# Performance work log

Hardware: AMD Instinct MI355X
Metric: run time of the kernel (lower is better)

Reference implementation:

```python
import jax, jax.numpy as jnp
import numpy as np

C = 256
CQK = C // 8  # query/key projection dim


def setup_inputs() -> dict:
    key = jax.random.key(0)
    ks = jax.random.split(key, 8)
    B, H, W = 4, 64, 64
    x = jax.random.normal(ks[0], (B, C, H, W), dtype=jnp.float32)
    # 1x1 Conv1d == per-position linear: weight [out, in], bias [out]
    Wq = jax.random.normal(ks[1], (CQK, C), dtype=jnp.float32) * (1.0 / np.sqrt(C))
    bq = jax.random.normal(ks[2], (CQK,), dtype=jnp.float32) * 0.01
    Wk = jax.random.normal(ks[3], (CQK, C), dtype=jnp.float32) * (1.0 / np.sqrt(C))
    bk = jax.random.normal(ks[4], (CQK,), dtype=jnp.float32) * 0.01
    Wv = jax.random.normal(ks[5], (C, C), dtype=jnp.float32) * (1.0 / np.sqrt(C))
    bv = jax.random.normal(ks[6], (C,), dtype=jnp.float32) * 0.01
    gamma = jax.random.normal(ks[7], (1,), dtype=jnp.float32) * 0.1
    return {"x": x, "Wq": Wq, "bq": bq, "Wk": Wk, "bk": bk,
            "Wv": Wv, "bv": bv, "gamma": gamma}


def reference(x, Wq, bq, Wk, bk, Wv, bv, gamma):
    B, Cc, H, W = x.shape
    xf = x.reshape(B, Cc, H * W)                      # [B, C, N]
    q = jnp.einsum('oc,bcn->bon', Wq, xf) + bq[:, None]   # [B, C/8, N]
    k = jnp.einsum('oc,bcn->bon', Wk, xf) + bk[:, None]   # [B, C/8, N]
    v = jnp.einsum('oc,bcn->bon', Wv, xf) + bv[:, None]   # [B, C,   N]
    # energy = q^T k  (unscaled, SAGAN-style)
    energy = jnp.einsum('bon,bom->bnm', q, k)              # [B, N, N]
    attn = jax.nn.softmax(energy, axis=-1)                 # rows over key dim
    # out = value @ attention^T
    out = jnp.einsum('bcm,bnm->bcn', v, attn)              # [B, C, N]
    out = out.reshape(B, Cc, H, W)
    return gamma * out + x
```

## Files before the change

### kernel.cpp

```cpp
#include <hip/hip_runtime.h>
#include <hip/hip_bf16.h>
#include <math.h>
#include <stdint.h>

#define N_POS 4096
#define C_DIM 256
#define CQK_D 32
#define NSPLIT 3

typedef __attribute__((ext_vector_type(8))) short bf16x8;
typedef __attribute__((ext_vector_type(4))) float f32x4;
typedef __attribute__((ext_vector_type(4))) uint32_t u32x4;

__device__ inline uint16_t f2bf(float f){
  union { __hip_bfloat16 h; uint16_t u; } c;
  c.h = __float2bfloat16(f);
  return c.u;
}
__device__ inline uint32_t pk2bf(float a, float b){
  union { __hip_bfloat162 h; uint32_t u; } c;
  c.h = __float22bfloat162_rn(float2{a, b});
  return c.u;
}
__device__ inline float bf2f_lo(uint32_t d){ return __uint_as_float(d << 16); }
__device__ inline float bf2f_hi(uint32_t d){ return __uint_as_float(d & 0xFFFF0000u); }

__global__ __launch_bounds__(256) void prep(
    const float* __restrict__ x,
    const float* __restrict__ Wq, const float* __restrict__ bq,
    const float* __restrict__ Wk, const float* __restrict__ bk,
    const float* __restrict__ Wv, const float* __restrict__ bv,
    ushort* __restrict__ xT_bf, ushort* __restrict__ W_bf, float* __restrict__ bias_f)
{
    const int tid = threadIdx.x;
    if (blockIdx.x == 64) {
        const int sub = blockIdx.z * 4 + blockIdx.y;
        const int e0 = sub * 5120;
        #pragma unroll
        for (int it = 0; it < 5; ++it) {
            const int e = e0 + (it*256 + tid)*4;
            const int o = e >> 8, c = e & 255;
            float4 w;
            if (o < 32)       w = *reinterpret_cast<const float4*>(&Wq[o*C_DIM + c]);
            else if (o < 64)  w = *reinterpret_cast<const float4*>(&Wk[(o-32)*C_DIM + c]);
            else              w = *reinterpret_cast<const float4*>(&Wv[(o-64)*C_DIM + c]);
            uint2 u; u.x = pk2bf(w.x, w.y); u.y = pk2bf(w.z, w.w);
            *reinterpret_cast<uint2*>(W_bf + e) = u;
        }
        if (sub == 0) {
            for (int i = tid; i < 320; i += 256)
                bias_f[i] = (i < 32) ? bq[i] : (i < 64) ? bk[i-32] : bv[i-64];
        }
        return;
    }
    __shared__ float t[64][65];
    const int jj4 = (tid & 15) * 4;
    const int rg  = tid >> 4;
    const int n0 = blockIdx.x * 64;
    const int c0 = blockIdx.y * 64;
    const int b  = blockIdx.z;
    #pragma unroll
    for (int ii = 0; ii < 4; ++ii) {
        const int cl = ii*16 + rg;
        const float4 xv = *reinterpret_cast<const float4*>(
            &x[((size_t)(b*C_DIM) + c0 + cl)*N_POS + n0 + jj4]);
        float* tr = &t[cl][jj4];
        tr[0] = xv.x; tr[1] = xv.y; tr[2] = xv.z; tr[3] = xv.w;
    }
    __syncthreads();
    #pragma unroll
    for (int ii = 0; ii < 8; ++ii) {
        const int flat = ii*256 + tid;
        const int nl = flat >> 5;
        const int cp = flat & 31;
        const uint32_t d = pk2bf(t[2*cp][nl], t[2*cp+1][nl]);
        *reinterpret_cast<uint32_t*>(xT_bf + ((size_t)(b*N_POS) + n0 + nl)*C_DIM + c0 + 2*cp) = d;
    }
}

__global__ __launch_bounds__(256, 4) void qkv_gemm(
    const ushort* __restrict__ xT_bf, const ushort* __restrict__ W_bf,
    const float* __restrict__ bias_f,
    ushort* __restrict__ q_bf, ushort* __restrict__ k_bf, ushort* __restrict__ v_bf)
{
    __shared__ ushort xs[64*C_DIM];
    const int tid  = threadIdx.x;
    const int wv   = tid >> 6;
    const int lane = tid & 63;
    const int g    = lane >> 4;
    const int q    = lane & 15;
    const int y    = blockIdx.y;
    const int b    = blockIdx.z;
    const int n0   = blockIdx.x * 64;

    {
        const char* xTb = (const char*)(xT_bf + ((size_t)(b*N_POS) + n0)*C_DIM);
        const int n_l    = (tid*16) >> 9;
        const int inner  = (tid & 31) << 4;
        #pragma unroll
        for (int s = 0; s < 8; ++s) {
            const int n = s*8 + n_l;
            const int src_inner = inner ^ ((n & 7) << 4);
            __builtin_amdgcn_global_load_lds(
                (const __attribute__((address_space(1))) uint32_t*)(xTb + (size_t)n*512 + src_inner),
                (__attribute__((address_space(3))) uint32_t*)((char*)xs + s*4096 + wv*1024),
                16, 0, 0);
        }
    }
    __syncthreads();

    f32x4 zero4 = {0.f,0.f,0.f,0.f};
    f32x4 acc[5];
    #pragma unroll
    for (int i = 0; i < 5; ++i) acc[i] = zero4;

    const char* xrow = (const char*)xs + (wv*16 + q)*512;
    const int sw = (q & 7) << 4;

    #pragma unroll
    for (int kk = 0; kk < 8; ++kk) {
        const bf16x8 xf = *reinterpret_cast<const bf16x8*>(xrow + ((kk*64 + g*16) ^ sw));
        const ushort* wrow = W_bf + (y*80 + q)*C_DIM + kk*32 + g*8;
        #pragma unroll
        for (int i = 0; i < 5; ++i) {
            const bf16x8 wf = *reinterpret_cast<const bf16x8*>(wrow + i*16*C_DIM);
            acc[i] = __builtin_amdgcn_mfma_f32_16x16x32_bf16(wf, xf, acc[i], 0, 0, 0);
        }
    }

    const int n = n0 + wv*16 + q;
    #pragma unroll
    for (int i = 0; i < 5; ++i) {
        const int got = y*5 + i;
        const int ob  = got*16 + 4*g;
        const float4 bi = *reinterpret_cast<const float4*>(bias_f + ob);
        if (got < 4) {
            const uint32_t u0 = pk2bf(acc[i][0] + bi.x, acc[i][1] + bi.y);
            const uint32_t u1 = pk2bf(acc[i][2] + bi.z, acc[i][3] + bi.w);
            ushort* dst = (got < 2 ? q_bf : k_bf) + ((size_t)(b*N_POS) + n)*CQK_D + (ob & 31);
            uint2 u; u.x = u0; u.y = u1;
            *reinterpret_cast<uint2*>(dst) = u;
        } else {
            const int c = ob - 64;
            ushort* vB = v_bf + (size_t)(b*C_DIM)*N_POS + n;
            vB[(size_t)(c+0)*N_POS] = f2bf(acc[i][0] + bi.x);
            vB[(size_t)(c+1)*N_POS] = f2bf(acc[i][1] + bi.y);
            vB[(size_t)(c+2)*N_POS] = f2bf(acc[i][2] + bi.z);
            vB[(size_t)(c+3)*N_POS] = f2bf(acc[i][3] + bi.w);
        }
    }
}

__global__ __launch_bounds__(256, 3) void flash_mfma(
    const ushort* __restrict__ q_bf, const ushort* __restrict__ k_bf,
    const ushort* __restrict__ v_bf, ushort* __restrict__ o_part,
    float* __restrict__ lsum)
{
    __shared__ ushort vt[C_DIM*64];
    __shared__ ushort pt[2][4*16*64];
    __shared__ float  l_s[64];

    const int tid  = threadIdx.x;
    const int wv   = tid >> 6;
    const int lane = tid & 63;
    const int g    = lane >> 4;
    const int q    = lane & 15;
    const int half = blockIdx.y;
    const int b    = blockIdx.z;
    const int n0   = blockIdx.x * 64;
    const int qrow = n0 + wv*16 + q;
    const int mt0  = (half == 0) ? 0 : 22 + (half-1)*21;
    const int mt1  = mt0 + ((half == 0) ? 22 : 21);

    const ushort* qb = q_bf + (size_t)b*N_POS*CQK_D;
    const ushort* kb = k_bf + (size_t)b*N_POS*CQK_D;
    const ushort* vb = v_bf + (size_t)b*C_DIM*N_POS;

    const bf16x8 qfrag = *reinterpret_cast<const bf16x8*>(qb + (size_t)qrow*CQK_D + g*8);

    f32x4 zero4 = {0.f, 0.f, 0.f, 0.f};
    f32x4 acc[4][4];
    #pragma unroll
    for (int i = 0; i < 4; ++i)
        #pragma unroll
        for (int j = 0; j < 4; ++j) acc[i][j] = zero4;
    float l = 0.f;

    const int swq = (q & 7) << 4;
    const int st_hi = lane >> 3, st_lo = lane & 7;
    const ushort* vsrc0 = vb + (size_t)(wv*64 + st_hi)*N_POS + st_lo*8;
    char* vdst0 = (char*)vt + (wv*64 + st_hi)*128 + (((st_lo ^ st_hi) & 7) << 4);

    auto loadK = [&](int mtx, bf16x8* kf) {
        const int mm = mtx * 64;
        #pragma unroll
        for (int t = 0; t < 4; ++t)
            kf[t] = *reinterpret_cast<const bf16x8*>(kb + (size_t)(mm + t*16 + q)*CQK_D + g*8);
    };

    auto chunk = [&](int mtx, bf16x8* kfc, bf16x8* kfn, int pfmt) {
        const int m0 = mtx * 64;
        const int buf = mtx & 1;
        char* ptw = (char*)pt[buf] + wv*2048;

        u32x4 vreg[8];
        #pragma unroll
        for (int s = 0; s < 8; ++s)
            vreg[s] = *reinterpret_cast<const u32x4*>(vsrc0 + (size_t)s*8*N_POS + m0);

        f32x4 sv[4];
        #pragma unroll
        for (int t = 0; t < 4; ++t)
            sv[t] = __builtin_amdgcn_mfma_f32_16x16x32_bf16(kfc[t], qfrag, zero4, 0, 0, 0);

        uint32_t pk[8];
        float psum = 0.f;
        #pragma unroll
        for (int t = 0; t < 4; ++t) {
            const float p0 = __expf(sv[t][0]), p1 = __expf(sv[t][1]);
            const float p2 = __expf(sv[t][2]), p3 = __expf(sv[t][3]);
            psum += (p0+p1)+(p2+p3);
            pk[2*t]   = pk2bf(p0, p1);
            pk[2*t+1] = pk2bf(p2, p3);
        }
        psum += __shfl_xor(psum, 16);
        psum += __shfl_xor(psum, 32);
        l += psum;

        #pragma unroll
        for (int t = 0; t < 4; ++t) {
            const int a = q*128 + ((t*32 + g*8) ^ swq);
            uint2 u; u.x = pk[2*t]; u.y = pk[2*t+1];
            *reinterpret_cast<uint2*>(ptw + a) = u;
        }
        #pragma unroll
        for (int s = 0; s < 8; ++s)
            *reinterpret_cast<u32x4*>(vdst0 + s*1024) = vreg[s];

        loadK(pfmt, kfn);

        __syncthreads();

        bf16x8 vf[8];
        #pragma unroll
        for (int ct = 0; ct < 4; ++ct)
            #pragma unroll
            for (int mm = 0; mm < 2; ++mm)
                vf[ct*2+mm] = *reinterpret_cast<const bf16x8*>(
                    (char*)vt + (wv*64 + ct*16 + q)*128 + ((mm*64 + g*16) ^ swq));

        __builtin_amdgcn_s_setprio(1);
        #pragma unroll
        for (int mm = 0; mm < 2; ++mm) {
            #pragma unroll
            for (int qt = 0; qt < 4; ++qt) {
                const bf16x8 pb = *reinterpret_cast<const bf16x8*>(
                    (char*)pt[buf] + qt*2048 + q*128 + ((mm*64 + g*16) ^ swq));
                #pragma unroll
                for (int ct = 0; ct < 4; ++ct)
                    acc[ct][qt] = __builtin_amdgcn_mfma_f32_16x16x32_bf16(vf[ct*2+mm], pb, acc[ct][qt], 0, 0, 0);
            }
        }
        __builtin_amdgcn_s_setprio(0);
    };

    bf16x8 kfA[4], kfB[4];
    loadK(mt0, kfA);
    int mt = mt0;
    for (; mt + 1 < mt1; mt += 2) {
        chunk(mt,   kfA, kfB, mt + 1);
        chunk(mt+1, kfB, kfA, (mt + 2 < mt1) ? mt + 2 : mt1 - 1);
    }
    if (mt < mt1) chunk(mt, kfA, kfB, mt);

    if (g == 0)
        lsum[(size_t)((half*4 + b)*N_POS) + qrow] = l;

    if (g == 0) l_s[wv*16 + q] = l;
    __syncthreads();
    float invl[4];
    #pragma unroll
    for (int qt = 0; qt < 4; ++qt) invl[qt] = 1.f / l_s[qt*16 + q];

    char* obase = (char*)o_part + ((size_t)((half*4 + b)*N_POS) + n0)*512;
    #pragma unroll
    for (int qt = 0; qt < 4; ++qt) {
        char* orow = obase + (size_t)(qt*16 + q)*512 + (wv*64 + 4*g)*2;
        #pragma unroll
        for (int ct = 0; ct < 4; ++ct) {
            const uint32_t u0 = pk2bf(acc[ct][qt][0]*invl[qt], acc[ct][qt][1]*invl[qt]);
            const uint32_t u1 = pk2bf(acc[ct][qt][2]*invl[qt], acc[ct][qt][3]*invl[qt]);
            uint2 u; u.x = u0; u.y = u1;
            *reinterpret_cast<uint2*>(orow + ct*32) = u;
        }
    }
}

__global__ __launch_bounds__(256) void out_combine(
    const ushort* __restrict__ o_part, const float* __restrict__ lsum,
    const float* __restrict__ x, const float* __restrict__ gamma,
    float* __restrict__ out)
{
    __shared__ float t[64][65];
    __shared__ float w0s[64], w1s[64], w2s[64];
    const int tid = threadIdx.x;
    const int nt = blockIdx.x;
    const int ct = blockIdx.y;
    const int b  = blockIdx.z;
    const int n0 = nt*64, c0 = ct*64;
    const float gm = gamma[0];

    if (tid < 64) {
        const float e0 = lsum[(size_t)((0*4 + b)*N_POS) + n0 + tid];
        const float e1 = lsum[(size_t)((1*4 + b)*N_POS) + n0 + tid];
        const float e2 = lsum[(size_t)((2*4 + b)*N_POS) + n0 + tid];
        const float inv = 1.f / (e0 + e1 + e2);
        w0s[tid] = e0 * inv;
        w1s[tid] = e1 * inv;
        w2s[tid] = e2 * inv;
    }
    __syncthreads();

    #pragma unroll
    for (int ii = 0; ii < 2; ++ii) {
        const int item = ii*256 + tid;
        const int nl = item >> 3;
        const int oc = item & 7;
        const size_t off = ((size_t)(b*N_POS) + n0 + nl)*C_DIM + c0 + oc*8;
        const uint4 d0 = *reinterpret_cast<const uint4*>(o_part + off);
        const uint4 d1 = *reinterpret_cast<const uint4*>(o_part + (size_t)4*N_POS*C_DIM + off);
        const uint4 d2 = *reinterpret_cast<const uint4*>(o_part + (size_t)8*N_POS*C_DIM + off);
        const float w0 = w0s[nl], w1 = w1s[nl], w2 = w2s[nl];
        float* tr = &t[nl][oc*8];
        tr[0] = w0*bf2f_lo(d0.x) + w1*bf2f_lo(d1.x) + w2*bf2f_lo(d2.x);
        tr[1] = w0*bf2f_hi(d0.x) + w1*bf2f_hi(d1.x) + w2*bf2f_hi(d2.x);
        tr[2] = w0*bf2f_lo(d0.y) + w1*bf2f_lo(d1.y) + w2*bf2f_lo(d2.y);
        tr[3] = w0*bf2f_hi(d0.y) + w1*bf2f_hi(d1.y) + w2*bf2f_hi(d2.y);
        tr[4] = w0*bf2f_lo(d0.z) + w1*bf2f_lo(d1.z) + w2*bf2f_lo(d2.z);
        tr[5] = w0*bf2f_hi(d0.z) + w1*bf2f_hi(d1.z) + w2*bf2f_hi(d2.z);
        tr[6] = w0*bf2f_lo(d0.w) + w1*bf2f_lo(d1.w) + w2*bf2f_lo(d2.w);
        tr[7] = w0*bf2f_hi(d0.w) + w1*bf2f_hi(d1.w) + w2*bf2f_hi(d2.w);
    }
    __syncthreads();
    {
        const int jj4 = (tid & 15) * 4;
        const int cg  = tid >> 4;
        #pragma unroll
        for (int ii = 0; ii < 4; ++ii) {
            const int cl = ii*16 + cg;
            const size_t idx = ((size_t)(b*C_DIM) + c0 + cl)*N_POS + n0 + jj4;
            const float4 xv = *reinterpret_cast<const float4*>(&x[idx]);
            float4 o;
            o.x = gm * t[jj4+0][cl] + xv.x;
            o.y = gm * t[jj4+1][cl] + xv.y;
            o.z = gm * t[jj4+2][cl] + xv.z;
            o.w = gm * t[jj4+3][cl] + xv.w;
            *reinterpret_cast<float4*>(&out[idx]) = o;
        }
    }
}

extern "C" void kernel_launch(void* const* d_in, const int* in_sizes, int n_in,
                              void* d_out, int out_size, void* d_ws, size_t ws_size,
                              hipStream_t stream)
{
    const float* x     = (const float*)d_in[0];
    const float* Wq    = (const float*)d_in[1];
    const float* bq    = (const float*)d_in[2];
    const float* Wk    = (const float*)d_in[3];
    const float* bk    = (const float*)d_in[4];
    const float* Wv    = (const float*)d_in[5];
    const float* bv    = (const float*)d_in[6];
    const float* gamma = (const float*)d_in[7];

    ushort* o_part = (ushort*)d_ws;
    ushort* xT_bf  = (ushort*)d_ws;
    float*  lsum   = (float*)(o_part + (size_t)NSPLIT*4*N_POS*C_DIM);
    ushort* q_bf   = (ushort*)(lsum + (size_t)NSPLIT*4*N_POS);
    ushort* k_bf   = q_bf + (size_t)4*N_POS*CQK_D;
    ushort* v_bf   = k_bf + (size_t)4*N_POS*CQK_D;
    ushort* W_bf   = v_bf + (size_t)4*C_DIM*N_POS;
    float*  bias_f = (float*)(W_bf + 320*C_DIM);
    float* out = (float*)d_out;

    prep<<<dim3(65,4,4), 256, 0, stream>>>(x, Wq, bq, Wk, bk, Wv, bv, xT_bf, W_bf, bias_f);
    qkv_gemm<<<dim3(64,4,4), 256, 0, stream>>>(xT_bf, W_bf, bias_f, q_bf, k_bf, v_bf);
    flash_mfma<<<dim3(64,NSPLIT,4), 256, 0, stream>>>(q_bf, k_bf, v_bf, o_part, lsum);
    out_combine<<<dim3(64,4,4), 256, 0, stream>>>(o_part, lsum, x, gamma, out);
}
```

Measured before the change: 95.97 us.

## Fuse x transpose and bf16 conversion into QKV GEMM kernel

The separate prep pass that transposed x to a bf16 [N,C] buffer in global memory is removed, and each qkv_gemm block now loads its fp32 x tile directly and transposes it through a padded LDS buffer into the swizzled bf16 layout. Weight conversion moves to a small standalone kernel. This drops a global write and re-read of the transposed activations. In exchange, the blockIdx.y groups each redo the same transpose of their x tile, LDS per block grows, and occupancy drops from 4 to 3 blocks per CU.

```diff
diff --git a/kernel.cpp b/kernel.cpp
--- a/kernel.cpp
+++ b/kernel.cpp
@@ -25,65 +25,35 @@
 __device__ inline float bf2f_lo(uint32_t d){ return __uint_as_float(d << 16); }
 __device__ inline float bf2f_hi(uint32_t d){ return __uint_as_float(d & 0xFFFF0000u); }
 
-__global__ __launch_bounds__(256) void prep(
-    const float* __restrict__ x,
+__global__ __launch_bounds__(256) void prep_w(
     const float* __restrict__ Wq, const float* __restrict__ bq,
     const float* __restrict__ Wk, const float* __restrict__ bk,
     const float* __restrict__ Wv, const float* __restrict__ bv,
-    ushort* __restrict__ xT_bf, ushort* __restrict__ W_bf, float* __restrict__ bias_f)
+    ushort* __restrict__ W_bf, float* __restrict__ bias_f)
 {
     const int tid = threadIdx.x;
-    if (blockIdx.x == 64) {
-        const int sub = blockIdx.z * 4 + blockIdx.y;
-        const int e0 = sub * 5120;
-        #pragma unroll
-        for (int it = 0; it < 5; ++it) {
-            const int e = e0 + (it*256 + tid)*4;
-            const int o = e >> 8, c = e & 255;
-            float4 w;
-            if (o < 32)       w = *reinterpret_cast<const float4*>(&Wq[o*C_DIM + c]);
-            else if (o < 64)  w = *reinterpret_cast<const float4*>(&Wk[(o-32)*C_DIM + c]);
-            else              w = *reinterpret_cast<const float4*>(&Wv[(o-64)*C_DIM + c]);
-            uint2 u; u.x = pk2bf(w.x, w.y); u.y = pk2bf(w.z, w.w);
-            *reinterpret_cast<uint2*>(W_bf + e) = u;
-        }
-        if (sub == 0) {
-            for (int i = tid; i < 320; i += 256)
-                bias_f[i] = (i < 32) ? bq[i] : (i < 64) ? bk[i-32] : bv[i-64];
-        }
+    if (blockIdx.x == 80) {
+        for (int i = tid; i < 320; i += 256)
+            bias_f[i] = (i < 32) ? bq[i] : (i < 64) ? bk[i-32] : bv[i-64];
         return;
     }
-    __shared__ float t[64][65];
-    const int jj4 = (tid & 15) * 4;
-    const int rg  = tid >> 4;
-    const int n0 = blockIdx.x * 64;
-    const int c0 = blockIdx.y * 64;
-    const int b  = blockIdx.z;
-    #pragma unroll
-    for (int ii = 0; ii < 4; ++ii) {
-        const int cl = ii*16 + rg;
-        const float4 xv = *reinterpret_cast<const float4*>(
-            &x[((size_t)(b*C_DIM) + c0 + cl)*N_POS + n0 + jj4]);
-        float* tr = &t[cl][jj4];
-        tr[0] = xv.x; tr[1] = xv.y; tr[2] = xv.z; tr[3] = xv.w;
-    }
-    __syncthreads();
-    #pragma unroll
-    for (int ii = 0; ii < 8; ++ii) {
-        const int flat = ii*256 + tid;
-        const int nl = flat >> 5;
-        const int cp = flat & 31;
-        const uint32_t d = pk2bf(t[2*cp][nl], t[2*cp+1][nl]);
-        *reinterpret_cast<uint32_t*>(xT_bf + ((size_t)(b*N_POS) + n0 + nl)*C_DIM + c0 + 2*cp) = d;
-    }
-}
-
-__global__ __launch_bounds__(256, 4) void qkv_gemm(
-    const ushort* __restrict__ xT_bf, const ushort* __restrict__ W_bf,
+    const int e = blockIdx.x * 1024 + tid * 4;
+    const int o = e >> 8, c = e & 255;
+    float4 w;
+    if (o < 32)       w = *reinterpret_cast<const float4*>(&Wq[o*C_DIM + c]);
+    else if (o < 64)  w = *reinterpret_cast<const float4*>(&Wk[(o-32)*C_DIM + c]);
+    else              w = *reinterpret_cast<const float4*>(&Wv[(o-64)*C_DIM + c]);
+    uint2 u; u.x = pk2bf(w.x, w.y); u.y = pk2bf(w.z, w.w);
+    *reinterpret_cast<uint2*>(W_bf + e) = u;
+}
+
+__global__ __launch_bounds__(256, 3) void qkv_gemm(
+    const float* __restrict__ x, const ushort* __restrict__ W_bf,
     const float* __restrict__ bias_f,
     ushort* __restrict__ q_bf, ushort* __restrict__ k_bf, ushort* __restrict__ v_bf)
 {
     __shared__ ushort xs[64*C_DIM];
+    __shared__ float  t[64][65];
     const int tid  = threadIdx.x;
     const int wv   = tid >> 6;
     const int lane = tid & 63;
@@ -94,20 +64,31 @@
     const int n0   = blockIdx.x * 64;
 
     {
-        const char* xTb = (const char*)(xT_bf + ((size_t)(b*N_POS) + n0)*C_DIM);
-        const int n_l    = (tid*16) >> 9;
-        const int inner  = (tid & 31) << 4;
-        #pragma unroll
-        for (int s = 0; s < 8; ++s) {
-            const int n = s*8 + n_l;
-            const int src_inner = inner ^ ((n & 7) << 4);
-            __builtin_amdgcn_global_load_lds(
-                (const __attribute__((address_space(1))) uint32_t*)(xTb + (size_t)n*512 + src_inner),
-                (__attribute__((address_space(3))) uint32_t*)((char*)xs + s*4096 + wv*1024),
-                16, 0, 0);
-        }
-    }
-    __syncthreads();
+        const float* xb = x + (size_t)(b*C_DIM)*N_POS + n0;
+        const int jj4 = (tid & 15) * 4;
+        const int rg  = tid >> 4;
+        for (int slab = 0; slab < 4; ++slab) {
+            #pragma unroll
+            for (int ii = 0; ii < 4; ++ii) {
+                const int cl = ii*16 + rg;
+                const float4 xv = *reinterpret_cast<const float4*>(
+                    xb + (size_t)(slab*64 + cl)*N_POS + jj4);
+                float* tr = &t[cl][jj4];
+                tr[0] = xv.x; tr[1] = xv.y; tr[2] = xv.z; tr[3] = xv.w;
+            }
+            __syncthreads();
+            #pragma unroll
+            for (int ii = 0; ii < 8; ++ii) {
+                const int flat = ii*256 + tid;
+                const int nl = flat >> 5;
+                const int cp = flat & 31;
+                const uint32_t d = pk2bf(t[2*cp][nl], t[2*cp+1][nl]);
+                *reinterpret_cast<uint32_t*>(
+                    (char*)xs + nl*512 + ((slab*128 + cp*4) ^ ((nl & 7) << 4))) = d;
+            }
+            __syncthreads();
+        }
+    }
 
     f32x4 zero4 = {0.f,0.f,0.f,0.f};
     f32x4 acc[5];
@@ -374,7 +355,6 @@
     const float* gamma = (const float*)d_in[7];
 
     ushort* o_part = (ushort*)d_ws;
-    ushort* xT_bf  = (ushort*)d_ws;
     float*  lsum   = (float*)(o_part + (size_t)NSPLIT*4*N_POS*C_DIM);
     ushort* q_bf   = (ushort*)(lsum + (size_t)NSPLIT*4*N_POS);
     ushort* k_bf   = q_bf + (size_t)4*N_POS*CQK_D;
@@ -383,8 +363,8 @@
     float*  bias_f = (float*)(W_bf + 320*C_DIM);
     float* out = (float*)d_out;
 
-    prep<<<dim3(65,4,4), 256, 0, stream>>>(x, Wq, bq, Wk, bk, Wv, bv, xT_bf, W_bf, bias_f);
-    qkv_gemm<<<dim3(64,4,4), 256, 0, stream>>>(xT_bf, W_bf, bias_f, q_bf, k_bf, v_bf);
+    prep_w<<<dim3(81), 256, 0, stream>>>(Wq, bq, Wk, bk, Wv, bv, W_bf, bias_f);
+    qkv_gemm<<<dim3(64,4,4), 256, 0, stream>>>(x, W_bf, bias_f, q_bf, k_bf, v_bf);
     flash_mfma<<<dim3(64,NSPLIT,4), 256, 0, stream>>>(q_bf, k_bf, v_bf, o_part, lsum);
     out_combine<<<dim3(64,4,4), 256, 0, stream>>>(o_part, lsum, x, gamma, out);
 }
```

New measurement: 108.6 us. 1.13x slower.

## Halve V LDS tile and use four-way key split for higher occupancy

Applied to the files above, without the earlier changes.

The V staging buffer in LDS is cut in half. V is now written and read in two phases within each chunk, which frees LDS so four blocks can share a CU (launch bounds raised from 3 to 4). The key range is split four ways instead of three when the workspace is large enough, giving 1024 blocks. The combine kernel now loops over a runtime split count. In exchange, each chunk gets an extra LDS write/read phase that is not fenced by a barrier. The combine kernel also reads one more bf16 partial buffer.

```diff
diff --git a/kernel.cpp b/kernel.cpp
--- a/kernel.cpp
+++ b/kernel.cpp
@@ -6,7 +6,6 @@
 #define N_POS 4096
 #define C_DIM 256
 #define CQK_D 32
-#define NSPLIT 3
 
 typedef __attribute__((ext_vector_type(8))) short bf16x8;
 typedef __attribute__((ext_vector_type(4))) float f32x4;
@@ -151,12 +150,12 @@
     }
 }
 
-__global__ __launch_bounds__(256, 3) void flash_mfma(
+__global__ __launch_bounds__(256, 4) void flash_mfma(
     const ushort* __restrict__ q_bf, const ushort* __restrict__ k_bf,
     const ushort* __restrict__ v_bf, ushort* __restrict__ o_part,
-    float* __restrict__ lsum)
+    float* __restrict__ lsum, int nsplit)
 {
-    __shared__ ushort vt[C_DIM*64];
+    __shared__ ushort vt[C_DIM*32];
     __shared__ ushort pt[2][4*16*64];
     __shared__ float  l_s[64];
 
@@ -169,8 +168,9 @@
     const int b    = blockIdx.z;
     const int n0   = blockIdx.x * 64;
     const int qrow = n0 + wv*16 + q;
-    const int mt0  = (half == 0) ? 0 : 22 + (half-1)*21;
-    const int mt1  = mt0 + ((half == 0) ? 22 : 21);
+    int mt0, mt1;
+    if (nsplit == 4) { mt0 = half*16; mt1 = mt0 + 16; }
+    else { mt0 = (half == 0) ? 0 : 22 + (half-1)*21; mt1 = mt0 + ((half == 0) ? 22 : 21); }
 
     const ushort* qb = q_bf + (size_t)b*N_POS*CQK_D;
     const ushort* kb = k_bf + (size_t)b*N_POS*CQK_D;
@@ -189,7 +189,7 @@
     const int swq = (q & 7) << 4;
     const int st_hi = lane >> 3, st_lo = lane & 7;
     const ushort* vsrc0 = vb + (size_t)(wv*64 + st_hi)*N_POS + st_lo*8;
-    char* vdst0 = (char*)vt + (wv*64 + st_hi)*128 + (((st_lo ^ st_hi) & 7) << 4);
+    char* vdst0 = (char*)vt + wv*4096 + st_hi*128 + (((st_lo ^ st_hi) & 7) << 4);
 
     auto loadK = [&](int mtx, bf16x8* kf) {
         const int mm = mtx * 64;
@@ -234,7 +234,7 @@
             *reinterpret_cast<uint2*>(ptw + a) = u;
         }
         #pragma unroll
-        for (int s = 0; s < 8; ++s)
+        for (int s = 0; s < 4; ++s)
             *reinterpret_cast<u32x4*>(vdst0 + s*1024) = vreg[s];
 
         loadK(pfmt, kfn);
@@ -243,11 +243,20 @@
 
         bf16x8 vf[8];
         #pragma unroll
-        for (int ct = 0; ct < 4; ++ct)
+        for (int ct = 0; ct < 2; ++ct)
             #pragma unroll
             for (int mm = 0; mm < 2; ++mm)
                 vf[ct*2+mm] = *reinterpret_cast<const bf16x8*>(
-                    (char*)vt + (wv*64 + ct*16 + q)*128 + ((mm*64 + g*16) ^ swq));
+                    (char*)vt + wv*4096 + (ct*16 + q)*128 + ((mm*64 + g*16) ^ swq));
+        #pragma unroll
+        for (int s = 0; s < 4; ++s)
+            *reinterpret_cast<u32x4*>(vdst0 + s*1024) = vreg[4+s];
+        #pragma unroll
+        for (int ct = 2; ct < 4; ++ct)
+            #pragma unroll
+            for (int mm = 0; mm < 2; ++mm)
+                vf[ct*2+mm] = *reinterpret_cast<const bf16x8*>(
+                    (char*)vt + wv*4096 + ((ct-2)*16 + q)*128 + ((mm*64 + g*16) ^ swq));
 
         __builtin_amdgcn_s_setprio(1);
         #pragma unroll
@@ -299,25 +308,28 @@
 __global__ __launch_bounds__(256) void out_combine(
     const ushort* __restrict__ o_part, const float* __restrict__ lsum,
     const float* __restrict__ x, const float* __restrict__ gamma,
-    float* __restrict__ out)
+    float* __restrict__ out, int nsplit)
 {
     __shared__ float t[64][65];
-    __shared__ float w0s[64], w1s[64], w2s[64];
+    __shared__ float w_s[4][64];
     const int tid = threadIdx.x;
     const int nt = blockIdx.x;
     const int ct = blockIdx.y;
     const int b  = blockIdx.z;
     const int n0 = nt*64, c0 = ct*64;
     const float gm = gamma[0];
+    const size_t SPLIT = (size_t)4*N_POS*C_DIM;
 
     if (tid < 64) {
-        const float e0 = lsum[(size_t)((0*4 + b)*N_POS) + n0 + tid];
-        const float e1 = lsum[(size_t)((1*4 + b)*N_POS) + n0 + tid];
-        const float e2 = lsum[(size_t)((2*4 + b)*N_POS) + n0 + tid];
-        const float inv = 1.f / (e0 + e1 + e2);
-        w0s[tid] = e0 * inv;
-        w1s[tid] = e1 * inv;
-        w2s[tid] = e2 * inv;
+        float e[4];
+        float sum = 0.f;
+        for (int s = 0; s < nsplit; ++s) {
+            e[s] = lsum[(size_t)((s*4 + b)*N_POS) + n0 + tid];
+            sum += e[s];
+        }
+        const float inv = 1.f / sum;
+        for (int s = 0; s < nsplit; ++s)
+            w_s[s][tid] = e[s] * inv;
     }
     __syncthreads();
 
@@ -327,19 +339,17 @@
         const int nl = item >> 3;
         const int oc = item & 7;
         const size_t off = ((size_t)(b*N_POS) + n0 + nl)*C_DIM + c0 + oc*8;
-        const uint4 d0 = *reinterpret_cast<const uint4*>(o_part + off);
-        const uint4 d1 = *reinterpret_cast<const uint4*>(o_part + (size_t)4*N_POS*C_DIM + off);
-        const uint4 d2 = *reinterpret_cast<const uint4*>(o_part + (size_t)8*N_POS*C_DIM + off);
-        const float w0 = w0s[nl], w1 = w1s[nl], w2 = w2s[nl];
+        float a0=0.f,a1=0.f,a2=0.f,a3=0.f,a4=0.f,a5=0.f,a6=0.f,a7=0.f;
+        for (int s = 0; s < nsplit; ++s) {
+            const uint4 d = *reinterpret_cast<const uint4*>(o_part + s*SPLIT + off);
+            const float w = w_s[s][nl];
+            a0 += w*bf2f_lo(d.x); a1 += w*bf2f_hi(d.x);
+            a2 += w*bf2f_lo(d.y); a3 += w*bf2f_hi(d.y);
+            a4 += w*bf2f_lo(d.z); a5 += w*bf2f_hi(d.z);
+            a6 += w*bf2f_lo(d.w); a7 += w*bf2f_hi(d.w);
+        }
         float* tr = &t[nl][oc*8];
-        tr[0] = w0*bf2f_lo(d0.x) + w1*bf2f_lo(d1.x) + w2*bf2f_lo(d2.x);
-        tr[1] = w0*bf2f_hi(d0.x) + w1*bf2f_hi(d1.x) + w2*bf2f_hi(d2.x);
-        tr[2] = w0*bf2f_lo(d0.y) + w1*bf2f_lo(d1.y) + w2*bf2f_lo(d2.y);
-        tr[3] = w0*bf2f_hi(d0.y) + w1*bf2f_hi(d1.y) + w2*bf2f_hi(d2.y);
-        tr[4] = w0*bf2f_lo(d0.z) + w1*bf2f_lo(d1.z) + w2*bf2f_lo(d2.z);
-        tr[5] = w0*bf2f_hi(d0.z) + w1*bf2f_hi(d1.z) + w2*bf2f_hi(d2.z);
-        tr[6] = w0*bf2f_lo(d0.w) + w1*bf2f_lo(d1.w) + w2*bf2f_lo(d2.w);
-        tr[7] = w0*bf2f_hi(d0.w) + w1*bf2f_hi(d1.w) + w2*bf2f_hi(d2.w);
+        tr[0]=a0; tr[1]=a1; tr[2]=a2; tr[3]=a3; tr[4]=a4; tr[5]=a5; tr[6]=a6; tr[7]=a7;
     }
     __syncthreads();
     {
@@ -373,10 +383,15 @@
     const float* bv    = (const float*)d_in[6];
     const float* gamma = (const float*)d_in[7];
 
+    const size_t need4 =
+        (size_t)4*4*N_POS*C_DIM*2 + (size_t)4*4*N_POS*4 +
+        (size_t)4*N_POS*CQK_D*2*2 + (size_t)4*C_DIM*N_POS*2 + 320*C_DIM*2 + 320*4;
+    const int ns = (ws_size >= need4) ? 4 : 3;
+
     ushort* o_part = (ushort*)d_ws;
     ushort* xT_bf  = (ushort*)d_ws;
-    float*  lsum   = (float*)(o_part + (size_t)NSPLIT*4*N_POS*C_DIM);
-    ushort* q_bf   = (ushort*)(lsum + (size_t)NSPLIT*4*N_POS);
+    float*  lsum   = (float*)(o_part + (size_t)ns*4*N_POS*C_DIM);
+    ushort* q_bf   = (ushort*)(lsum + (size_t)ns*4*N_POS);
     ushort* k_bf   = q_bf + (size_t)4*N_POS*CQK_D;
     ushort* v_bf   = k_bf + (size_t)4*N_POS*CQK_D;
     ushort* W_bf   = v_bf + (size_t)4*C_DIM*N_POS;
@@ -385,6 +400,6 @@
 
     prep<<<dim3(65,4,4), 256, 0, stream>>>(x, Wq, bq, Wk, bk, Wv, bv, xT_bf, W_bf, bias_f);
     qkv_gemm<<<dim3(64,4,4), 256, 0, stream>>>(xT_bf, W_bf, bias_f, q_bf, k_bf, v_bf);
-    flash_mfma<<<dim3(64,NSPLIT,4), 256, 0, stream>>>(q_bf, k_bf, v_bf, o_part, lsum);
-    out_combine<<<dim3(64,4,4), 256, 0, stream>>>(o_part, lsum, x, gamma, out);
-}
+    flash_mfma<<<dim3(64,ns,4), 256, 0, stream>>>(q_bf, k_bf, v_bf, o_part, lsum, ns);
+    out_combine<<<dim3(64,4,4), 256, 0, stream>>>(o_part, lsum, x, gamma, out, ns);
+}
```

New measurement: 293.8 us. +206.2%, slower.
